# Optimization experiments

Hardware: AMD Instinct MI355X
Metric: run time of the kernel (lower is better)

## Reference

```python
import jax, jax.numpy as jnp
import numpy as np

H, D_MODEL, D_K, D_V = 16, 1024, 64, 64
IS_DECODE = True


def setup_inputs() -> dict:
    key = jax.random.key(0)
    ks = jax.random.split(key, 6)
    N, L = 4, 2048
    x = jax.random.normal(ks[0], (N, L, D_MODEL), dtype=jnp.float32)
    masked_info = jnp.ones((N, L), dtype=jnp.float32)  # 1 = valid, 0 = pad
    s = 1.0 / np.sqrt(D_MODEL)
    WQ = jax.random.normal(ks[1], (H, D_MODEL, D_K), dtype=jnp.float32) * s
    WK = jax.random.normal(ks[2], (H, D_MODEL, D_K), dtype=jnp.float32) * s
    WV = jax.random.normal(ks[3], (H, D_MODEL, D_V), dtype=jnp.float32) * s
    WO = jax.random.normal(ks[4], (H * D_V, D_MODEL), dtype=jnp.float32) * s
    return {"x": x, "masked_info": masked_info, "WQ": WQ, "WK": WK, "WV": WV, "WO": WO}


def reference(x, masked_info, WQ, WK, WV, WO):
    N, L, _ = x.shape
    scaler = jnp.sqrt(jnp.array(D_K, dtype=x.dtype))
    # per-head projections, batched over heads: [H, N, L, d]
    q = jnp.einsum('nld,hdk->hnlk', x, WQ)
    k = jnp.einsum('nld,hdk->hnlk', x, WK)
    v = jnp.einsum('nld,hdv->hnlv', x, WV)
    scores = jnp.einsum('hnlk,hnmk->hnlm', q, k) / scaler  # [H, N, L, L]
    # outer-product padding mask: True where masked out
    pad_mask = (masked_info[:, :, None] * masked_info[:, None, :]) == 0  # [N, L, L]
    if IS_DECODE:
        causal = jnp.triu(jnp.ones((L, L), dtype=bool), k=1)
        pad_mask = pad_mask | causal[None, :, :]
    scores = jnp.where(pad_mask[None], -jnp.inf, scores)
    attn = jax.nn.softmax(scores, axis=-1)
    attn = jnp.nan_to_num(attn, nan=0.0)  # rows fully masked -> 0
    out_h = jnp.einsum('hnlm,hnmv->hnlv', attn, v)  # [H, N, L, d_v]
    # concat heads along last dim in head order: [N, L, H*d_v]
    concat = jnp.transpose(out_h, (1, 2, 0, 3)).reshape(N, L, H * D_V)
    return concat @ WO
```

## Files before the change

kernel.cpp:

```cpp
#include <hip/hip_runtime.h>
#include <hip/hip_bf16.h>


typedef unsigned short ushort_t;
typedef __bf16 bf16x8 __attribute__((ext_vector_type(8)));
typedef float  f32x4  __attribute__((ext_vector_type(4)));
typedef unsigned short us4 __attribute__((ext_vector_type(4)));
typedef short s16x4 __attribute__((ext_vector_type(4)));

__device__ __forceinline__ ushort_t f2bf(float f) {
    union { float f; unsigned u; } a; a.f = f;
    unsigned r = a.u + 0x7fffu + ((a.u >> 16) & 1u);
    return (ushort_t)(r >> 16);
}

__device__ __forceinline__ void gload16(const ushort_t* g, ushort_t* l) {
    __builtin_amdgcn_global_load_lds(
        (const __attribute__((address_space(1))) void*)g,
        (__attribute__((address_space(3))) void*)l, 16, 0, 0);
}

__global__ __launch_bounds__(256) void cvt_f32_bf16(const float* __restrict__ in,
                                                    ushort_t* __restrict__ out, int n4) {
    int i = blockIdx.x * 256 + threadIdx.x;
    if (i >= n4) return;
    float4 v = reinterpret_cast<const float4*>(in)[i];
    us4 o;
    o[0] = f2bf(v.x); o[1] = f2bf(v.y); o[2] = f2bf(v.z); o[3] = f2bf(v.w);
    reinterpret_cast<us4*>(out)[i] = o;
}

__global__ __launch_bounds__(256) void cvt_transpose32(const float* __restrict__ in,
                                                       ushort_t* __restrict__ out,
                                                       int R, int C) {
    const int b = blockIdx.z;
    const int c0 = blockIdx.x * 32, r0 = blockIdx.y * 32;
    const int tx = threadIdx.x & 31, ty = threadIdx.x >> 5;
    __shared__ ushort_t t[32][33];
    const float* ip = in + ((size_t)b * R + r0) * C + c0;
    #pragma unroll
    for (int i = 0; i < 4; ++i)
        t[ty + 8 * i][tx] = f2bf(ip[(size_t)(ty + 8 * i) * C + tx]);
    __syncthreads();
    ushort_t* op = out + ((size_t)b * C + c0) * R + r0;
    #pragma unroll
    for (int i = 0; i < 4; ++i)
        op[(size_t)(ty + 8 * i) * R + tx] = t[tx][ty + 8 * i];
}

template<int MODE>
__global__ __launch_bounds__(256, 2)
void gemm_bt(const ushort_t* __restrict__ Ag, const ushort_t* __restrict__ BT,
             void* __restrict__ Cout, float scale) {
    const int bm = blockIdx.x, by = blockIdx.y;
    const int tid = threadIdx.x;
    const int w = tid >> 6, lane = tid & 63;
    const int wr = w >> 1, wc = w & 1;
    const int g = lane >> 4, c = lane & 15;
    const int m0 = bm * 128;
    const ushort_t* Bbase = BT + (size_t)by * 131072;

    __shared__ __align__(16) ushort_t As[128 * 64];
    __shared__ __align__(16) ushort_t Bs[128 * 64];

    f32x4 acc[4][4];
    #pragma unroll
    for (int i = 0; i < 4; ++i)
        #pragma unroll
        for (int j = 0; j < 4; ++j) acc[i][j] = (f32x4){0.f, 0.f, 0.f, 0.f};

    const int rsub = (w << 3) + (lane >> 3);
    const int s8   = lane & 7;

    for (int t = 0; t < 16; ++t) {
        const int k0 = t * 64;
        #pragma unroll
        for (int is = 0; is < 4; ++is) {
            const int row = is * 32 + rsub;
            const int sg  = (s8 ^ (row & 7)) << 3;
            gload16(Ag + (size_t)(m0 + row) * 1024 + k0 + sg, &As[is * 2048 + w * 512]);
            gload16(Bbase + (size_t)row * 1024 + k0 + sg,     &Bs[is * 2048 + w * 512]);
        }
        __syncthreads();
        #pragma unroll
        for (int kk = 0; kk < 2; ++kk) {
            bf16x8 af[4], bfr[4];
            #pragma unroll
            for (int mf = 0; mf < 4; ++mf) {
                const int row = wr * 64 + mf * 16 + c;
                const int slot = (kk * 4 + g) ^ (row & 7);
                af[mf] = *reinterpret_cast<const bf16x8*>(&As[row * 64 + slot * 8]);
            }
            #pragma unroll
            for (int nf = 0; nf < 4; ++nf) {
                const int row = wc * 64 + nf * 16 + c;
                const int slot = (kk * 4 + g) ^ (row & 7);
                bfr[nf] = *reinterpret_cast<const bf16x8*>(&Bs[row * 64 + slot * 8]);
            }
            __builtin_amdgcn_s_setprio(1);
            #pragma unroll
            for (int mf = 0; mf < 4; ++mf)
                #pragma unroll
                for (int nf = 0; nf < 4; ++nf)
                    acc[mf][nf] = __builtin_amdgcn_mfma_f32_16x16x32_bf16(
                        af[mf], bfr[nf], acc[mf][nf], 0, 0, 0);
            __builtin_amdgcn_s_setprio(0);
        }
        __syncthreads();
    }

    #pragma unroll
    for (int mf = 0; mf < 4; ++mf) {
        const int mbase = m0 + wr * 64 + mf * 16 + g * 4;
        #pragma unroll
        for (int nf = 0; nf < 4; ++nf) {
            const int colG = wc * 64 + nf * 16 + c;
            if (MODE == 3) {
                const int s  = by * 2 + (colG >> 6);
                const int c2 = colG & 63;
                ushort_t* o = (ushort_t*)Cout + (size_t)s * 524288;
                if (s < 32) {
                    const float scl = (s < 16) ? scale : 1.0f;
                    #pragma unroll
                    for (int r = 0; r < 4; ++r)
                        o[(size_t)(mbase + r) * 64 + c2] = f2bf(acc[mf][nf][r] * scl);
                } else {
                    us4 pk;
                    #pragma unroll
                    for (int r = 0; r < 4; ++r) pk[r] = f2bf(acc[mf][nf][r]);
                    const int nIdx = mbase >> 11, l = mbase & 2047;
                    *reinterpret_cast<us4*>(
                        &o[(size_t)nIdx * 131072 + (size_t)c2 * 2048 + l]) = pk;
                }
            } else {
                float* o = (float*)Cout;
                #pragma unroll
                for (int r = 0; r < 4; ++r)
                    o[(size_t)(mbase + r) * 1024 + by * 128 + colG] = acc[mf][nf][r];
            }
        }
    }
}

__global__ __launch_bounds__(256, 4)
void attn_kernel(const ushort_t* __restrict__ qb, const ushort_t* __restrict__ kb,
                 const ushort_t* __restrict__ vtb, const float* __restrict__ mi,
                 ushort_t* __restrict__ cat) {
    const int bx = blockIdx.x;
    const int n = blockIdx.y, h = blockIdx.z;
    const int tid = threadIdx.x;
    const int w = tid >> 6, lane = tid & 63;
    const int g = lane >> 4, c = lane & 15;
    const int qblkA = bx, qblkB = 31 - bx;
    const int q0A = qblkA * 64 + w * 16;
    const int q0B = qblkB * 64 + w * 16;

    const ushort_t* qhn = qb  + (size_t)h * 524288 + (size_t)n * 131072;
    const ushort_t* khn = kb  + (size_t)h * 524288 + (size_t)n * 131072;
    const ushort_t* vhn = vtb + (size_t)h * 524288 + (size_t)n * 131072;
    const float*    mrow = mi + (size_t)n * 2048;

    __shared__ __align__(16) ushort_t Ks[2][64 * 64];
    __shared__ __align__(16) ushort_t Vs[2][64 * 64];

    const int rsub = (w << 3) + (lane >> 3);
    const int s8   = lane & 7;

    auto stage = [&](int jb, int b) {
        const int kbase = jb * 64;
        #pragma unroll
        for (int is = 0; is < 2; ++is) {
            const int row = is * 32 + rsub;
            const int sg  = (s8 ^ (row & 7)) << 3;
            gload16(khn + (size_t)(kbase + row) * 64 + sg, &Ks[b][is * 2048 + w * 512]);
            gload16(vhn + (size_t)row * 2048 + kbase + sg, &Vs[b][is * 2048 + w * 512]);
        }
    };

    bf16x8 qfA[2], qfB[2];
    {
        const ushort_t* qa = qhn + (size_t)(q0A + c) * 64 + g * 8;
        const ushort_t* qb2 = qhn + (size_t)(q0B + c) * 64 + g * 8;
        qfA[0] = *reinterpret_cast<const bf16x8*>(qa);
        qfA[1] = *reinterpret_cast<const bf16x8*>(qa + 32);
        qfB[0] = *reinterpret_cast<const bf16x8*>(qb2);
        qfB[1] = *reinterpret_cast<const bf16x8*>(qb2 + 32);
    }
    const float mqA = mrow[q0A + c];
    const float mqB = mrow[q0B + c];

    float mrunA = -1e30f, lrunA = 0.f, mrunB = -1e30f, lrunB = 0.f;
    f32x4 accA[4], accB[4];
    #pragma unroll
    for (int i = 0; i < 4; ++i) {
        accA[i] = (f32x4){0.f, 0.f, 0.f, 0.f};
        accB[i] = (f32x4){0.f, 0.f, 0.f, 0.f};
    }

    stage(0, 0);
    __syncthreads();
    int buf = 0;

    for (int j = 0; j <= qblkB; ++j) {
        if (j < qblkB) stage(j + 1, buf ^ 1);
        const int kbase = j * 64;
        f32x4 bias[4];
        #pragma unroll
        for (int nf = 0; nf < 4; ++nf) {
            float4 mk = *reinterpret_cast<const float4*>(&mrow[kbase + nf * 16 + g * 4]);
            bias[nf][0] = (mk.x == 0.f) ? -1e30f : 0.f;
            bias[nf][1] = (mk.y == 0.f) ? -1e30f : 0.f;
            bias[nf][2] = (mk.z == 0.f) ? -1e30f : 0.f;
            bias[nf][3] = (mk.w == 0.f) ? -1e30f : 0.f;
        }

        auto do_pass = [&](const bf16x8* qf, f32x4* acc, float& mrun, float& lrun,
                           int q0, bool diag) {
            f32x4 s[4];
            #pragma unroll
            for (int nf = 0; nf < 4; ++nf) s[nf] = (f32x4){0.f, 0.f, 0.f, 0.f};
            __builtin_amdgcn_s_setprio(1);
            #pragma unroll
            for (int kk = 0; kk < 2; ++kk)
                #pragma unroll
                for (int nf = 0; nf < 4; ++nf) {
                    const int row  = nf * 16 + c;
                    const int byte = row * 128 + (((kk * 4 + g) ^ (c & 7)) << 4);
                    bf16x8 kf = *reinterpret_cast<const bf16x8*>(
                        reinterpret_cast<const char*>(&Ks[buf][0]) + byte);
                    s[nf] = __builtin_amdgcn_mfma_f32_16x16x32_bf16(
                        kf, qf[kk], s[nf], 0, 0, 0);
                }
            __builtin_amdgcn_s_setprio(0);
            #pragma unroll
            for (int nf = 0; nf < 4; ++nf) s[nf] += bias[nf];
            if (diag) {
                const int qrow = q0 + c;
                #pragma unroll
                for (int nf = 0; nf < 4; ++nf)
                    #pragma unroll
                    for (int r = 0; r < 4; ++r)
                        if (kbase + nf * 16 + g * 4 + r > qrow) s[nf][r] = -1e30f;
            }
            float m01[4], m23[4];
            #pragma unroll
            for (int r = 0; r < 4; ++r) {
                m01[r] = fmaxf(s[0][r], s[1][r]);
                m23[r] = fmaxf(s[2][r], s[3][r]);
            }
            float mt = fmaxf(fmaxf(fmaxf(m01[0], m01[1]), fmaxf(m01[2], m01[3])),
                             fmaxf(fmaxf(m23[0], m23[1]), fmaxf(m23[2], m23[3])));
            mt = fmaxf(mt, __shfl_xor(mt, 16));
            mt = fmaxf(mt, __shfl_xor(mt, 32));
            if (!__all(mt - mrun <= 8.0f)) {
                const float mnew = fmaxf(mrun, mt);
                const float sc = __builtin_amdgcn_exp2f(mrun - mnew);
                #pragma unroll
                for (int nfd = 0; nfd < 4; ++nfd)
                    #pragma unroll
                    for (int r = 0; r < 4; ++r) acc[nfd][r] *= sc;
                lrun *= sc;
                mrun = mnew;
            }
            float rs = 0.f;
            union { unsigned u[2]; s16x4 v; } pb[4];
            #pragma unroll
            for (int nf = 0; nf < 4; ++nf) {
                const float p0 = __builtin_amdgcn_exp2f(s[nf][0] - mrun);
                const float p1 = __builtin_amdgcn_exp2f(s[nf][1] - mrun);
                const float p2 = __builtin_amdgcn_exp2f(s[nf][2] - mrun);
                const float p3 = __builtin_amdgcn_exp2f(s[nf][3] - mrun);
                rs += (p0 + p1) + (p2 + p3);
                asm("v_cvt_pk_bf16_f32 %0, %1, %2" : "=v"(pb[nf].u[0]) : "v"(p0), "v"(p1));
                asm("v_cvt_pk_bf16_f32 %0, %1, %2" : "=v"(pb[nf].u[1]) : "v"(p2), "v"(p3));
            }
            rs += __shfl_xor(rs, 16);
            rs += __shfl_xor(rs, 32);
            lrun += rs;
            __builtin_amdgcn_s_setprio(1);
            #pragma unroll
            for (int kk = 0; kk < 4; ++kk)
                #pragma unroll
                for (int nfd = 0; nfd < 4; ++nfd) {
                    const int row   = nfd * 16 + c;
                    const int chunk = (kk * 2 + (g >> 1)) ^ (c & 7);
                    const int byte  = row * 128 + (chunk << 4) + (g & 1) * 8;
                    s16x4 vf = *reinterpret_cast<const s16x4*>(
                        reinterpret_cast<const char*>(&Vs[buf][0]) + byte);
                    acc[nfd] = __builtin_amdgcn_mfma_f32_16x16x16bf16_1k(
                        vf, pb[kk].v, acc[nfd], 0, 0, 0);
                }
            __builtin_amdgcn_s_setprio(0);
        };

        if (j <= qblkA) do_pass(qfA, accA, mrunA, lrunA, q0A, j == qblkA);
        do_pass(qfB, accB, mrunB, lrunB, q0B, j == qblkB);

        __syncthreads();
        buf ^= 1;
    }

    auto epi = [&](const f32x4* acc, float mrun, float lrun, float mq, int q0) {
        const float inv = (mq != 0.f && mrun > -1e29f && lrun > 0.f)
                              ? (1.0f / lrun) : 0.f;
        const size_t base = (size_t)(n * 2048 + q0 + c) * 1024 + h * 64;
        #pragma unroll
        for (int nfd = 0; nfd < 4; ++nfd) {
            us4 pk;
            #pragma unroll
            for (int r = 0; r < 4; ++r) pk[r] = f2bf(acc[nfd][r] * inv);
            *reinterpret_cast<us4*>(&cat[base + nfd * 16 + g * 4]) = pk;
        }
    };
    epi(accA, mrunA, lrunA, mqA, q0A);
    epi(accB, mrunB, lrunB, mqB, q0B);
}

extern "C" void kernel_launch(void* const* d_in, const int* in_sizes, int n_in,
                              void* d_out, int out_size, void* d_ws, size_t ws_size,
                              hipStream_t stream) {
    const float* x  = (const float*)d_in[0];
    const float* mi = (const float*)d_in[1];
    const float* WQ = (const float*)d_in[2];
    const float* WK = (const float*)d_in[3];
    const float* WV = (const float*)d_in[4];
    const float* WO = (const float*)d_in[5];
    float* out = (float*)d_out;

    ushort_t* ws  = (ushort_t*)d_ws;
    ushort_t* xb  = ws;
    ushort_t* wqt = xb  + 8388608;
    ushort_t* wkt = wqt + 1048576;
    ushort_t* wvt = wkt + 1048576;
    ushort_t* wot = wvt + 1048576;
    ushort_t* qb  = wot + 1048576;
    ushort_t* kb  = qb  + 8388608;
    ushort_t* vtb = kb  + 8388608;
    ushort_t* cat = xb;

    cvt_f32_bf16<<<8192, 256, 0, stream>>>(x, xb, 2097152);
    {
        dim3 gt(2, 32, 16);
        cvt_transpose32<<<gt, 256, 0, stream>>>(WQ, wqt, 1024, 64);
        cvt_transpose32<<<gt, 256, 0, stream>>>(WK, wkt, 1024, 64);
        cvt_transpose32<<<gt, 256, 0, stream>>>(WV, wvt, 1024, 64);
        dim3 go(32, 32, 1);
        cvt_transpose32<<<go, 256, 0, stream>>>(WO, wot, 1024, 1024);
    }

    dim3 g1(64, 24);
    gemm_bt<3><<<g1, 256, 0, stream>>>(xb, wqt, qb, 0.18033688f);

    dim3 g2(16, 4, 16);
    attn_kernel<<<g2, 256, 0, stream>>>(qb, kb, vtb, mi, cat);

    dim3 g3(64, 8);
    gemm_bt<2><<<g3, 256, 0, stream>>>(cat, wot, out, 1.0f);
}
```

Baseline: 193.1 us.

## Share K fragment loads across both query passes, remap attention blocks to XCDs, fuse QKV weight transpose

The attention loop now loads each K fragment from LDS once and feeds it to the QK MFMAs of both query tiles (A and B), instead of reloading it inside each pass. The mask bias is used as the initial value of the score accumulator, and V fragments are batched before their MFMAs. The grid becomes a 1D launch whose block index is remapped so blocks sharing the same (head, batch) land on the same XCD for L2 reuse of K/V. The three QKV weight transposes are merged into one launch. In exchange, more score registers stay live at once, which may raise register pressure.

Result: slower. 200.6 us (+3.9%).

```diff
diff --git a/kernel.cpp b/kernel.cpp
--- a/kernel.cpp
+++ b/kernel.cpp
@@ -46,6 +46,27 @@
     #pragma unroll
     for (int i = 0; i < 4; ++i)
         op[(size_t)(ty + 8 * i) * R + tx] = t[tx][ty + 8 * i];
+}
+
+__global__ __launch_bounds__(256) void cvt_transpose_qkv(const float* __restrict__ WQ,
+                                                         const float* __restrict__ WK,
+                                                         const float* __restrict__ WV,
+                                                         ushort_t* __restrict__ out) {
+    const int z = blockIdx.z;
+    const float* in = (z < 16) ? WQ : (z < 32) ? WK : WV;
+    const int b = z & 15;
+    const int c0 = blockIdx.x * 32, r0 = blockIdx.y * 32;
+    const int tx = threadIdx.x & 31, ty = threadIdx.x >> 5;
+    __shared__ ushort_t t[32][33];
+    const float* ip = in + ((size_t)b * 1024 + r0) * 64 + c0;
+    #pragma unroll
+    for (int i = 0; i < 4; ++i)
+        t[ty + 8 * i][tx] = f2bf(ip[(size_t)(ty + 8 * i) * 64 + tx]);
+    __syncthreads();
+    ushort_t* op = out + (size_t)z * 65536 + (size_t)c0 * 1024 + r0;
+    #pragma unroll
+    for (int i = 0; i < 4; ++i)
+        op[(size_t)(ty + 8 * i) * 1024 + tx] = t[tx][ty + 8 * i];
 }
 
 template<int MODE>
@@ -146,8 +167,12 @@
 void attn_kernel(const ushort_t* __restrict__ qb, const ushort_t* __restrict__ kb,
                  const ushort_t* __restrict__ vtb, const float* __restrict__ mi,
                  ushort_t* __restrict__ cat) {
-    const int bx = blockIdx.x;
-    const int n = blockIdx.y, h = blockIdx.z;
+    const int bid = blockIdx.x;
+    const int xcd = bid & 7, slot = bid >> 3;
+    const int grp = ((slot & 7) << 3) | xcd;
+    const int bx  = slot >> 3;
+    const int h = grp >> 2, n = grp & 3;
+
     const int tid = threadIdx.x;
     const int w = tid >> 6, lane = tid & 63;
     const int g = lane >> 4, c = lane & 15;
@@ -201,100 +226,120 @@
     __syncthreads();
     int buf = 0;
 
+    auto softmax = [&](f32x4* s, f32x4* acc, float& mrun, float& lrun,
+                       bool diag, int q0, int kbase, unsigned* pb) {
+        if (diag) {
+            const int qrow = q0 + c;
+            #pragma unroll
+            for (int nf = 0; nf < 4; ++nf)
+                #pragma unroll
+                for (int r = 0; r < 4; ++r)
+                    if (kbase + nf * 16 + g * 4 + r > qrow) s[nf][r] = -1e30f;
+        }
+        float mm[4];
+        #pragma unroll
+        for (int r = 0; r < 4; ++r)
+            mm[r] = fmaxf(fmaxf(s[0][r], s[1][r]), fmaxf(s[2][r], s[3][r]));
+        float mt = fmaxf(fmaxf(mm[0], mm[1]), fmaxf(mm[2], mm[3]));
+        mt = fmaxf(mt, __shfl_xor(mt, 16));
+        mt = fmaxf(mt, __shfl_xor(mt, 32));
+        if (!__all(mt - mrun <= 8.0f)) {
+            const float mnew = fmaxf(mrun, mt);
+            const float sc = __builtin_amdgcn_exp2f(mrun - mnew);
+            #pragma unroll
+            for (int nfd = 0; nfd < 4; ++nfd)
+                #pragma unroll
+                for (int r = 0; r < 4; ++r) acc[nfd][r] *= sc;
+            lrun *= sc;
+            mrun = mnew;
+        }
+        float rs = 0.f;
+        #pragma unroll
+        for (int nf = 0; nf < 4; ++nf) {
+            const float p0 = __builtin_amdgcn_exp2f(s[nf][0] - mrun);
+            const float p1 = __builtin_amdgcn_exp2f(s[nf][1] - mrun);
+            const float p2 = __builtin_amdgcn_exp2f(s[nf][2] - mrun);
+            const float p3 = __builtin_amdgcn_exp2f(s[nf][3] - mrun);
+            rs += (p0 + p1) + (p2 + p3);
+            asm("v_cvt_pk_bf16_f32 %0, %1, %2" : "=v"(pb[nf * 2])     : "v"(p0), "v"(p1));
+            asm("v_cvt_pk_bf16_f32 %0, %1, %2" : "=v"(pb[nf * 2 + 1]) : "v"(p2), "v"(p3));
+        }
+        rs += __shfl_xor(rs, 16);
+        rs += __shfl_xor(rs, 32);
+        lrun += rs;
+    };
+
+    auto pv = [&](f32x4* acc, const unsigned* pb) {
+        __builtin_amdgcn_s_setprio(1);
+        #pragma unroll
+        for (int kk = 0; kk < 4; ++kk) {
+            union { unsigned u[2]; s16x4 v; } pu;
+            pu.u[0] = pb[kk * 2]; pu.u[1] = pb[kk * 2 + 1];
+            s16x4 vf[4];
+            #pragma unroll
+            for (int nfd = 0; nfd < 4; ++nfd) {
+                const int row   = nfd * 16 + c;
+                const int chunk = (kk * 2 + (g >> 1)) ^ (c & 7);
+                const int byt   = row * 128 + (chunk << 4) + (g & 1) * 8;
+                vf[nfd] = *reinterpret_cast<const s16x4*>(
+                    reinterpret_cast<const char*>(&Vs[buf][0]) + byt);
+            }
+            #pragma unroll
+            for (int nfd = 0; nfd < 4; ++nfd)
+                acc[nfd] = __builtin_amdgcn_mfma_f32_16x16x16bf16_1k(
+                    vf[nfd], pu.v, acc[nfd], 0, 0, 0);
+        }
+        __builtin_amdgcn_s_setprio(0);
+    };
+
     for (int j = 0; j <= qblkB; ++j) {
         if (j < qblkB) stage(j + 1, buf ^ 1);
         const int kbase = j * 64;
-        f32x4 bias[4];
+        const bool doA  = (j <= qblkA);
+        const bool diagA = (j == qblkA), diagB = (j == qblkB);
+
+        f32x4 sA[4], sB[4];
         #pragma unroll
         for (int nf = 0; nf < 4; ++nf) {
             float4 mk = *reinterpret_cast<const float4*>(&mrow[kbase + nf * 16 + g * 4]);
-            bias[nf][0] = (mk.x == 0.f) ? -1e30f : 0.f;
-            bias[nf][1] = (mk.y == 0.f) ? -1e30f : 0.f;
-            bias[nf][2] = (mk.z == 0.f) ? -1e30f : 0.f;
-            bias[nf][3] = (mk.w == 0.f) ? -1e30f : 0.f;
-        }
-
-        auto do_pass = [&](const bf16x8* qf, f32x4* acc, float& mrun, float& lrun,
-                           int q0, bool diag) {
-            f32x4 s[4];
-            #pragma unroll
-            for (int nf = 0; nf < 4; ++nf) s[nf] = (f32x4){0.f, 0.f, 0.f, 0.f};
-            __builtin_amdgcn_s_setprio(1);
-            #pragma unroll
-            for (int kk = 0; kk < 2; ++kk)
-                #pragma unroll
-                for (int nf = 0; nf < 4; ++nf) {
-                    const int row  = nf * 16 + c;
-                    const int byte = row * 128 + (((kk * 4 + g) ^ (c & 7)) << 4);
-                    bf16x8 kf = *reinterpret_cast<const bf16x8*>(
-                        reinterpret_cast<const char*>(&Ks[buf][0]) + byte);
-                    s[nf] = __builtin_amdgcn_mfma_f32_16x16x32_bf16(
-                        kf, qf[kk], s[nf], 0, 0, 0);
-                }
-            __builtin_amdgcn_s_setprio(0);
-            #pragma unroll
-            for (int nf = 0; nf < 4; ++nf) s[nf] += bias[nf];
-            if (diag) {
-                const int qrow = q0 + c;
+            f32x4 b;
+            b[0] = (mk.x == 0.f) ? -1e30f : 0.f;
+            b[1] = (mk.y == 0.f) ? -1e30f : 0.f;
+            b[2] = (mk.z == 0.f) ? -1e30f : 0.f;
+            b[3] = (mk.w == 0.f) ? -1e30f : 0.f;
+            sA[nf] = b; sB[nf] = b;
+        }
+        __builtin_amdgcn_s_setprio(1);
+        #pragma unroll
+        for (int kk = 0; kk < 2; ++kk) {
+            bf16x8 kf[4];
+            #pragma unroll
+            for (int nf = 0; nf < 4; ++nf) {
+                const int row = nf * 16 + c;
+                const int byt = row * 128 + (((kk * 4 + g) ^ (c & 7)) << 4);
+                kf[nf] = *reinterpret_cast<const bf16x8*>(
+                    reinterpret_cast<const char*>(&Ks[buf][0]) + byt);
+            }
+            if (doA) {
                 #pragma unroll
                 for (int nf = 0; nf < 4; ++nf)
-                    #pragma unroll
-                    for (int r = 0; r < 4; ++r)
-                        if (kbase + nf * 16 + g * 4 + r > qrow) s[nf][r] = -1e30f;
-            }
-            float m01[4], m23[4];
-            #pragma unroll
-            for (int r = 0; r < 4; ++r) {
-                m01[r] = fmaxf(s[0][r], s[1][r]);
-                m23[r] = fmaxf(s[2][r], s[3][r]);
-            }
-            float mt = fmaxf(fmaxf(fmaxf(m01[0], m01[1]), fmaxf(m01[2], m01[3])),
-                             fmaxf(fmaxf(m23[0], m23[1]), fmaxf(m23[2], m23[3])));
-            mt = fmaxf(mt, __shfl_xor(mt, 16));
-            mt = fmaxf(mt, __shfl_xor(mt, 32));
-            if (!__all(mt - mrun <= 8.0f)) {
-                const float mnew = fmaxf(mrun, mt);
-                const float sc = __builtin_amdgcn_exp2f(mrun - mnew);
-                #pragma unroll
-                for (int nfd = 0; nfd < 4; ++nfd)
-                    #pragma unroll
-                    for (int r = 0; r < 4; ++r) acc[nfd][r] *= sc;
-                lrun *= sc;
-                mrun = mnew;
-            }
-            float rs = 0.f;
-            union { unsigned u[2]; s16x4 v; } pb[4];
-            #pragma unroll
-            for (int nf = 0; nf < 4; ++nf) {
-                const float p0 = __builtin_amdgcn_exp2f(s[nf][0] - mrun);
-                const float p1 = __builtin_amdgcn_exp2f(s[nf][1] - mrun);
-                const float p2 = __builtin_amdgcn_exp2f(s[nf][2] - mrun);
-                const float p3 = __builtin_amdgcn_exp2f(s[nf][3] - mrun);
-                rs += (p0 + p1) + (p2 + p3);
-                asm("v_cvt_pk_bf16_f32 %0, %1, %2" : "=v"(pb[nf].u[0]) : "v"(p0), "v"(p1));
-                asm("v_cvt_pk_bf16_f32 %0, %1, %2" : "=v"(pb[nf].u[1]) : "v"(p2), "v"(p3));
-            }
-            rs += __shfl_xor(rs, 16);
-            rs += __shfl_xor(rs, 32);
-            lrun += rs;
-            __builtin_amdgcn_s_setprio(1);
-            #pragma unroll
-            for (int kk = 0; kk < 4; ++kk)
-                #pragma unroll
-                for (int nfd = 0; nfd < 4; ++nfd) {
-                    const int row   = nfd * 16 + c;
-                    const int chunk = (kk * 2 + (g >> 1)) ^ (c & 7);
-                    const int byte  = row * 128 + (chunk << 4) + (g & 1) * 8;
-                    s16x4 vf = *reinterpret_cast<const s16x4*>(
-                        reinterpret_cast<const char*>(&Vs[buf][0]) + byte);
-                    acc[nfd] = __builtin_amdgcn_mfma_f32_16x16x16bf16_1k(
-                        vf, pb[kk].v, acc[nfd], 0, 0, 0);
-                }
-            __builtin_amdgcn_s_setprio(0);
-        };
-
-        if (j <= qblkA) do_pass(qfA, accA, mrunA, lrunA, q0A, j == qblkA);
-        do_pass(qfB, accB, mrunB, lrunB, q0B, j == qblkB);
+                    sA[nf] = __builtin_amdgcn_mfma_f32_16x16x32_bf16(
+                        kf[nf], qfA[kk], sA[nf], 0, 0, 0);
+            }
+            #pragma unroll
+            for (int nf = 0; nf < 4; ++nf)
+                sB[nf] = __builtin_amdgcn_mfma_f32_16x16x32_bf16(
+                    kf[nf], qfB[kk], sB[nf], 0, 0, 0);
+        }
+        __builtin_amdgcn_s_setprio(0);
+
+        unsigned pbA[8], pbB[8];
+        if (doA) {
+            softmax(sA, accA, mrunA, lrunA, diagA, q0A, kbase, pbA);
+            pv(accA, pbA);
+        }
+        softmax(sB, accB, mrunB, lrunB, diagB, q0B, kbase, pbB);
+        pv(accB, pbB);
 
         __syncthreads();
         buf ^= 1;
@@ -330,9 +375,7 @@
     ushort_t* ws  = (ushort_t*)d_ws;
     ushort_t* xb  = ws;
     ushort_t* wqt = xb  + 8388608;
-    ushort_t* wkt = wqt + 1048576;
-    ushort_t* wvt = wkt + 1048576;
-    ushort_t* wot = wvt + 1048576;
+    ushort_t* wot = wqt + 3145728;
     ushort_t* qb  = wot + 1048576;
     ushort_t* kb  = qb  + 8388608;
     ushort_t* vtb = kb  + 8388608;
@@ -340,10 +383,8 @@
 
     cvt_f32_bf16<<<8192, 256, 0, stream>>>(x, xb, 2097152);
     {
-        dim3 gt(2, 32, 16);
-        cvt_transpose32<<<gt, 256, 0, stream>>>(WQ, wqt, 1024, 64);
-        cvt_transpose32<<<gt, 256, 0, stream>>>(WK, wkt, 1024, 64);
-        cvt_transpose32<<<gt, 256, 0, stream>>>(WV, wvt, 1024, 64);
+        dim3 gt(2, 32, 48);
+        cvt_transpose_qkv<<<gt, 256, 0, stream>>>(WQ, WK, WV, wqt);
         dim3 go(32, 32, 1);
         cvt_transpose32<<<go, 256, 0, stream>>>(WO, wot, 1024, 1024);
     }
@@ -351,8 +392,7 @@
     dim3 g1(64, 24);
     gemm_bt<3><<<g1, 256, 0, stream>>>(xb, wqt, qb, 0.18033688f);
 
-    dim3 g2(16, 4, 16);
-    attn_kernel<<<g2, 256, 0, stream>>>(qb, kb, vtb, mi, cat);
+    attn_kernel<<<1024, 256, 0, stream>>>(qb, kb, vtb, mi, cat);
 
     dim3 g3(64, 8);
     gemm_bt<2><<<g3, 256, 0, stream>>>(cat, wot, out, 1.0f);
```
